# Kernel tuning notes

Measured on AMD Instinct MI355X. Metric: run time of the kernel, lower is better.

## Reference

```python
import jax, jax.numpy as jnp
import numpy as np

B, L, D, H = 8, 4096, 512, 512  # batch, seq_len, input channels, hidden_dim
EPS = 1e-5


def setup_inputs() -> dict:
    key = jax.random.key(0)
    ks = jax.random.split(key, 6)
    sD = 1.0 / np.sqrt(D)
    sH = 1.0 / np.sqrt(H)
    return {
        "x": jax.random.normal(ks[0], (B, L, D), jnp.float32),
        "ln_gamma": jnp.ones((D,), jnp.float32),
        "ln_beta": jnp.zeros((D,), jnp.float32),
        "W_B": jax.random.normal(ks[1], (D, H), jnp.float32) * sD,
        "b_B": jnp.zeros((H,), jnp.float32),
        "W_C": jax.random.normal(ks[2], (D, H), jnp.float32) * sD,
        "b_C": jnp.zeros((H,), jnp.float32),
        "W_out": jax.random.normal(ks[3], (H, H), jnp.float32) * sH,
        "b_out": jnp.zeros((H,), jnp.float32),
        # original initializes A to zeros; use decays in (0,1) for a non-trivial scan
        "A": jax.random.uniform(ks[4], (H,), jnp.float32, 0.1, 0.95),
    }


def _scan_op(e1, e2):
    # composition of affine maps h -> a*h + b (elementwise, per channel)
    a1, b1 = e1
    a2, b2 = e2
    return a1 * a2, a2 * b1 + b2


def reference(x, ln_gamma, ln_beta, W_B, b_B, W_C, b_C, W_out, b_out, A):
    # LayerNorm over channels
    mu = jnp.mean(x, axis=-1, keepdims=True)
    var = jnp.var(x, axis=-1, keepdims=True)
    xn = (x - mu) * jax.lax.rsqrt(var + EPS) * ln_gamma + ln_beta  # [B,L,D]

    Bt = jnp.einsum("bld,dh->blh", xn, W_B) + b_B  # [B,L,H]
    Ct = jnp.einsum("bld,dh->blh", xn, W_C) + b_C  # [B,L,H]

    # linear recurrence h_t = A * h_{t-1} + B_t via associative scan over L
    a_full = jnp.broadcast_to(A, Bt.shape)
    _, h = jax.lax.associative_scan(_scan_op, (a_full, Bt), axis=1)  # [B,L,H]

    y = Ct * h  # selective readout
    return jnp.einsum("blh,ho->blo", y, W_out) + b_out  # [B,L,H]
```

## Files before the change

kernel.cpp:

```cpp
#include <hip/hip_runtime.h>
#include <hip/hip_bf16.h>
#include <stdint.h>

typedef __bf16 bf16x8 __attribute__((ext_vector_type(8)));
typedef float f32x4 __attribute__((ext_vector_type(4)));

constexpr int Bn = 8, Ln = 4096, Dn = 512, Hn = 512;
constexpr int Mrows = Bn * Ln;
constexpr int CHUNK = 64, NCHUNK = Ln / CHUNK;
constexpr int LNBLK = Mrows / 4;

__global__ __launch_bounds__(256) void pre_kernel(
    const float* __restrict__ x, const float* __restrict__ gamma,
    const float* __restrict__ beta,
    const float* __restrict__ W_B, const float* __restrict__ W_C,
    const float* __restrict__ W_out, const float* __restrict__ b_B,
    const float* __restrict__ b_C,
    __hip_bfloat16* __restrict__ xn,
    __hip_bfloat16* __restrict__ WbcT, __hip_bfloat16* __restrict__ WoT,
    float* __restrict__ bbc)
{
    int t = threadIdx.x;
    if (blockIdx.x >= LNBLK) {
        int id = (blockIdx.x - LNBLK) * 256 + t;
        {
            int n = id >> 9, k = id & 511;
            float wv = (n < Hn) ? W_B[k * Hn + n] : W_C[k * Hn + (n - Hn)];
            WbcT[id] = __float2bfloat16(wv);
        }
        if (id < Hn * Hn) {
            int n = id >> 9, k = id & 511;
            WoT[id] = __float2bfloat16(W_out[k * Hn + n]);
        }
        if (id < 2 * Hn) bbc[id] = (id < Hn) ? b_B[id] : b_C[id - Hn];
        return;
    }
    int wid = t >> 6, lane = t & 63;
    int blk = blockIdx.x;
    int row = (blk & 7) * Ln + (blk >> 3) * 4 + wid;
    const float4* xr = reinterpret_cast<const float4*>(x + (size_t)row * Dn);
    float4 pa = xr[lane], pb = xr[lane + 64];
    float s  = pa.x + pa.y + pa.z + pa.w + pb.x + pb.y + pb.z + pb.w;
    float s2 = pa.x * pa.x + pa.y * pa.y + pa.z * pa.z + pa.w * pa.w
             + pb.x * pb.x + pb.y * pb.y + pb.z * pb.z + pb.w * pb.w;
    #pragma unroll
    for (int off = 1; off < 64; off <<= 1) {
        s  += __shfl_xor(s, off);
        s2 += __shfl_xor(s2, off);
    }
    float mu = s * (1.0f / Dn);
    float var = s2 * (1.0f / Dn) - mu * mu;
    float inv = rsqrtf(var + 1e-5f);
    const float4* g4 = reinterpret_cast<const float4*>(gamma);
    const float4* b4 = reinterpret_cast<const float4*>(beta);
    float4 ga = g4[lane], gb = g4[lane + 64];
    float4 ba = b4[lane], bb = b4[lane + 64];
    __hip_bfloat16 o[8];
    o[0] = __float2bfloat16((pa.x - mu) * inv * ga.x + ba.x);
    o[1] = __float2bfloat16((pa.y - mu) * inv * ga.y + ba.y);
    o[2] = __float2bfloat16((pa.z - mu) * inv * ga.z + ba.z);
    o[3] = __float2bfloat16((pa.w - mu) * inv * ga.w + ba.w);
    o[4] = __float2bfloat16((pb.x - mu) * inv * gb.x + bb.x);
    o[5] = __float2bfloat16((pb.y - mu) * inv * gb.y + bb.y);
    o[6] = __float2bfloat16((pb.z - mu) * inv * gb.z + bb.z);
    o[7] = __float2bfloat16((pb.w - mu) * inv * gb.w + bb.w);
    ushort4* xo = reinterpret_cast<ushort4*>(xn + (size_t)row * Dn);
    xo[lane]      = *reinterpret_cast<ushort4*>(&o[0]);
    xo[lane + 64] = *reinterpret_cast<ushort4*>(&o[4]);
}

template <int NT, bool OUT_BF16, bool WRITE_S>
__global__ __launch_bounds__(256, 2) void gemm4_kernel(
    const __hip_bfloat16* __restrict__ A,
    const __hip_bfloat16* __restrict__ BT,
    const float* __restrict__ bias,
    void* __restrict__ Cout,
    const float* __restrict__ Av, float* __restrict__ Sout)
{
    constexpr int K = 512, NIT = 4;
    extern __shared__ unsigned short lds[];

    int nwg = gridDim.x, bid = blockIdx.x;
    int bswz = (bid & 7) * (nwg >> 3) + (bid >> 3);
    constexpr int NBN = NT / 128;
    int bm = bswz / NBN, bnb = bswz % NBN;
    int row0 = bm * 128, col0 = bnb * 128;

    int tid = threadIdx.x;
    int w = tid >> 6, l = tid & 63;
    int rl = l & 15, qg = l >> 4;

    int scol = ((l & 7) ^ (l >> 3)) * 8;
    const __hip_bfloat16* gA = A  + (size_t)(row0 + w * 16 + (l >> 3)) * K + scol;
    const __hip_bfloat16* gB = BT + (size_t)(col0 + w * 16 + (l >> 3)) * K + scol;

#define GLDS(src, dst) __builtin_amdgcn_global_load_lds( \
        (const __attribute__((address_space(1))) void*)(const void*)(src), \
        (__attribute__((address_space(3))) void*)(void*)(dst), 16, 0, 0)
#define STA(b, kt, h, sub) GLDS(gA + (size_t)((h) * 64 + (sub) * 8) * K + (kt) * 64, \
        &lds[(b) * 16384 + (h) * 4096 + w * 1024 + (sub) * 512])
#define STB(b, kt, h, sub) GLDS(gB + (size_t)((h) * 64 + (sub) * 8) * K + (kt) * 64, \
        &lds[(b) * 16384 + 8192 + (h) * 4096 + w * 1024 + (sub) * 512])
#define STAGE_AU(b, kt, h) { STA(b, kt, h, 0); STA(b, kt, h, 1); }
#define STAGE_BU(b, kt, h) { STB(b, kt, h, 0); STB(b, kt, h, 1); }
#define BARRIER { asm volatile("" ::: "memory"); __builtin_amdgcn_s_barrier(); \
                  asm volatile("" ::: "memory"); }
#define VMCNT(n) asm volatile("s_waitcnt vmcnt(" #n ")" ::: "memory")

    int aoff = ((w >> 1) * 64 + rl) * 64;
    int boff = 8192 + ((w & 1) * 64 + rl) * 64;
    int s0k0 = (qg ^ (rl & 7)) * 8;
    int s0k1 = ((4 + qg) ^ (rl & 7)) * 8;

    f32x4 acc[4][4] = {};
    bf16x8 af[2][2], bfr[4][2];

#define RD_A(mq, b) { _Pragma("unroll") for (int i2 = 0; i2 < 2; ++i2) { \
        af[i2][0] = *(const bf16x8*)&lds[(b) * 16384 + aoff + ((mq) * 32 + i2 * 16) * 64 + s0k0]; \
        af[i2][1] = *(const bf16x8*)&lds[(b) * 16384 + aoff + ((mq) * 32 + i2 * 16) * 64 + s0k1]; } }
#define RD_B(nq, b) { _Pragma("unroll") for (int j2 = 0; j2 < 2; ++j2) { \
        bfr[(nq) * 2 + j2][0] = *(const bf16x8*)&lds[(b) * 16384 + boff + ((nq) * 32 + j2 * 16) * 64 + s0k0]; \
        bfr[(nq) * 2 + j2][1] = *(const bf16x8*)&lds[(b) * 16384 + boff + ((nq) * 32 + j2 * 16) * 64 + s0k1]; } }
#define MM2(mq) { __builtin_amdgcn_s_setprio(1); \
        _Pragma("unroll") for (int nq = 0; nq < 2; ++nq) \
        _Pragma("unroll") for (int i2 = 0; i2 < 2; ++i2) \
        _Pragma("unroll") for (int j2 = 0; j2 < 2; ++j2) \
        _Pragma("unroll") for (int kk = 0; kk < 2; ++kk) \
            acc[(mq) * 2 + i2][nq * 2 + j2] = __builtin_amdgcn_mfma_f32_16x16x32_bf16( \
                af[i2][kk], bfr[nq * 2 + j2][kk], acc[(mq) * 2 + i2][nq * 2 + j2], 0, 0, 0); \
        __builtin_amdgcn_s_setprio(0); }

    STAGE_BU(0, 0, 0); STAGE_BU(0, 0, 1); STAGE_AU(0, 0, 0); STAGE_AU(0, 0, 1);
    STAGE_BU(1, 1, 0); STAGE_BU(1, 1, 1);
    VMCNT(4);
    BARRIER;

    for (int it = 0; it < NIT; ++it) {
        int e = 2 * it;
        bool more = (it < NIT - 1);
        RD_A(0, 0); RD_B(0, 0); RD_B(1, 0);
        STAGE_AU(1, e + 1, 0); STAGE_AU(1, e + 1, 1);
        BARRIER; MM2(0); BARRIER;
        RD_A(1, 0);
        if (more) { STAGE_BU(0, e + 2, 0); STAGE_BU(0, e + 2, 1); }
        BARRIER; MM2(1);
        if (more) { VMCNT(4); } else { VMCNT(0); }
        BARRIER;
        RD_A(0, 1); RD_B(0, 1); RD_B(1, 1);
        if (more) { STAGE_AU(0, e + 2, 0); STAGE_AU(0, e + 2, 1); }
        BARRIER; MM2(0); BARRIER;
        RD_A(1, 1);
        if (more) { STAGE_BU(1, e + 3, 0); STAGE_BU(1, e + 3, 1); }
        BARRIER; MM2(1);
        if (more) { VMCNT(4); BARRIER; }
    }

    int crow0 = row0 + (w >> 1) * 64 + qg * 4;
    int ccol0 = col0 + (w & 1) * 64 + rl;
    int cg = (row0 + (w >> 1) * 64) >> 6;
    float aCol[4];
    if (WRITE_S && col0 < 512) {
        #pragma unroll
        for (int n = 0; n < 4; ++n) aCol[n] = Av[ccol0 + n * 16];
    }
    #pragma unroll
    for (int n = 0; n < 4; ++n) {
        int col = ccol0 + n * 16;
        float bv = bias[col];
        float v[4][4];
        #pragma unroll
        for (int i = 0; i < 4; ++i) {
            #pragma unroll
            for (int j = 0; j < 4; ++j) {
                v[i][j] = acc[i][n][j] + bv;
                size_t idx = (size_t)(crow0 + i * 16 + j) * NT + col;
                if (OUT_BF16)
                    ((__hip_bfloat16*)Cout)[idx] = __float2bfloat16(v[i][j]);
                else
                    ((float*)Cout)[idx] = v[i][j];
            }
        }
        if (WRITE_S && col0 < 512) {
            float a = aCol[n];
            float a2 = a * a, a4 = a2 * a2, a8 = a4 * a4, a16 = a8 * a8;
            float s = 0.f;
            #pragma unroll
            for (int i = 0; i < 4; ++i) {
                float u = ((v[i][0] * a + v[i][1]) * a + v[i][2]) * a + v[i][3];
                s = s * a16 + u;
            }
            float aq = (qg == 0) ? a8 * a4 : (qg == 1) ? a8 : (qg == 2) ? a4 : 1.0f;
            s *= aq;
            s += __shfl_xor(s, 16);
            s += __shfl_xor(s, 32);
            if (qg == 0) Sout[(size_t)cg * Hn + col] = s;
        }
    }
#undef GLDS
#undef STA
#undef STB
#undef STAGE_AU
#undef STAGE_BU
#undef BARRIER
#undef VMCNT
#undef RD_A
#undef RD_B
#undef MM2
}

__global__ __launch_bounds__(256) void scan_kernel(
    const __hip_bfloat16* __restrict__ BC, const float* __restrict__ Av,
    const float* __restrict__ S, __hip_bfloat16* __restrict__ Y)
{
    int blk = blockIdx.x;
    int b = blk & 7;
    int half = (blk >> 3) & 1;
    int c = blk >> 4;
    int hh = half * 256 + threadIdx.x;
    float a = Av[hh];
    float aG = a;
    #pragma unroll
    for (int i = 0; i < 6; ++i) aG *= aG;
    float h = 0.f;
    const float* Sp = S + (size_t)b * NCHUNK * Hn + hh;
    for (int cc = 0; cc < c; ++cc)
        h = aG * h + Sp[(size_t)cc * Hn];
    const __hip_bfloat16* p = BC + ((size_t)(b * Ln + c * CHUNK) * 1024) + hh;
    __hip_bfloat16* yp = Y + ((size_t)(b * Ln + c * CHUNK) * Hn) + hh;
    #pragma unroll 8
    for (int i = 0; i < CHUNK; ++i) {
        float bv = __bfloat162float(p[(size_t)i * 1024]);
        float cv = __bfloat162float(p[(size_t)i * 1024 + 512]);
        h = a * h + bv;
        yp[(size_t)i * Hn] = __float2bfloat16(cv * h);
    }
}

extern "C" void kernel_launch(void* const* d_in, const int* in_sizes, int n_in,
                              void* d_out, int out_size, void* d_ws, size_t ws_size,
                              hipStream_t stream)
{
    const float* x     = (const float*)d_in[0];
    const float* ln_g  = (const float*)d_in[1];
    const float* ln_b  = (const float*)d_in[2];
    const float* W_B   = (const float*)d_in[3];
    const float* b_B   = (const float*)d_in[4];
    const float* W_C   = (const float*)d_in[5];
    const float* b_C   = (const float*)d_in[6];
    const float* W_out = (const float*)d_in[7];
    const float* b_out = (const float*)d_in[8];
    const float* Avec  = (const float*)d_in[9];

    char* ws = (char*)d_ws;
    __hip_bfloat16* WbcT = (__hip_bfloat16*)(ws);
    __hip_bfloat16* WoT  = (__hip_bfloat16*)(ws + (1u << 20));
    float*          bbc  = (float*)(ws + (1u << 20) + (1u << 19));
    __hip_bfloat16* XN   = (__hip_bfloat16*)(ws + (2u << 20));
    __hip_bfloat16* BC   = (__hip_bfloat16*)(ws + (34u << 20));
    float*          Sbuf = (float*)(ws + (98u << 20));
    __hip_bfloat16* Y    = (__hip_bfloat16*)(ws + (100u << 20));

    hipFuncSetAttribute((const void*)gemm4_kernel<1024, true, true>,
                        hipFuncAttributeMaxDynamicSharedMemorySize, 65536);
    hipFuncSetAttribute((const void*)gemm4_kernel<512, false, false>,
                        hipFuncAttributeMaxDynamicSharedMemorySize, 65536);

    pre_kernel<<<LNBLK + 2048, 256, 0, stream>>>(
        x, ln_g, ln_b, W_B, W_C, W_out, b_B, b_C, XN, WbcT, WoT, bbc);
    gemm4_kernel<1024, true, true><<<(Mrows / 128) * (1024 / 128), 256, 65536, stream>>>(
        XN, WbcT, bbc, BC, Avec, Sbuf);
    scan_kernel<<<Bn * NCHUNK * 2, 256, 0, stream>>>(BC, Avec, Sbuf, Y);
    gemm4_kernel<512, false, false><<<(Mrows / 128) * (512 / 128), 256, 65536, stream>>>(
        Y, WoT, b_out, d_out, nullptr, nullptr);
}
```

Measured before the change: 121.6 us.

## Switch GEMM to K=32 double-buffered tiles with 4 waves/SIMD occupancy

Replaces the K=64 half-tile staged GEMM pipeline with a simpler loop over K=32 tiles, double-buffered in 32 KB of LDS, with one read-all/MMA-all phase per step. Halving the LDS footprint and raising launch bounds to 4 blocks per CU is meant to hide latency through occupancy rather than intra-block software pipelining. The trade-off is fewer MFMAs per barrier (16 instead of 32), more barriers overall, and possible register pressure under the tighter launch bound.

```diff
diff --git a/kernel.cpp b/kernel.cpp
--- a/kernel.cpp
+++ b/kernel.cpp
@@ -70,14 +70,14 @@
 }
 
 template <int NT, bool OUT_BF16, bool WRITE_S>
-__global__ __launch_bounds__(256, 2) void gemm4_kernel(
+__global__ __launch_bounds__(256, 4) void gemm32_kernel(
     const __hip_bfloat16* __restrict__ A,
     const __hip_bfloat16* __restrict__ BT,
     const float* __restrict__ bias,
     void* __restrict__ Cout,
     const float* __restrict__ Av, float* __restrict__ Sout)
 {
-    constexpr int K = 512, NIT = 4;
+    constexpr int K = 512, NKT = 16;
     extern __shared__ unsigned short lds[];
 
     int nwg = gridDim.x, bid = blockIdx.x;
@@ -90,69 +90,56 @@
     int w = tid >> 6, l = tid & 63;
     int rl = l & 15, qg = l >> 4;
 
-    int scol = ((l & 7) ^ (l >> 3)) * 8;
-    const __hip_bfloat16* gA = A  + (size_t)(row0 + w * 16 + (l >> 3)) * K + scol;
-    const __hip_bfloat16* gB = BT + (size_t)(col0 + w * 16 + (l >> 3)) * K + scol;
+    int srow = l >> 2, sslot = l & 3;
+    int scol = (sslot ^ (srow & 3)) * 8;
+    const __hip_bfloat16* gA = A  + (size_t)(row0 + w * 32 + srow) * K + scol;
+    const __hip_bfloat16* gB = BT + (size_t)(col0 + w * 32 + srow) * K + scol;
 
 #define GLDS(src, dst) __builtin_amdgcn_global_load_lds( \
         (const __attribute__((address_space(1))) void*)(const void*)(src), \
         (__attribute__((address_space(3))) void*)(void*)(dst), 16, 0, 0)
-#define STA(b, kt, h, sub) GLDS(gA + (size_t)((h) * 64 + (sub) * 8) * K + (kt) * 64, \
-        &lds[(b) * 16384 + (h) * 4096 + w * 1024 + (sub) * 512])
-#define STB(b, kt, h, sub) GLDS(gB + (size_t)((h) * 64 + (sub) * 8) * K + (kt) * 64, \
-        &lds[(b) * 16384 + 8192 + (h) * 4096 + w * 1024 + (sub) * 512])
-#define STAGE_AU(b, kt, h) { STA(b, kt, h, 0); STA(b, kt, h, 1); }
-#define STAGE_BU(b, kt, h) { STB(b, kt, h, 0); STB(b, kt, h, 1); }
+#define STA(b, kt, s) GLDS(gA + (size_t)(s) * 16 * K + (kt) * 32, \
+        &lds[(b) * 8192 + w * 1024 + (s) * 512])
+#define STB(b, kt, s) GLDS(gB + (size_t)(s) * 16 * K + (kt) * 32, \
+        &lds[(b) * 8192 + 4096 + w * 1024 + (s) * 512])
+#define STAGE(b, kt) { STA(b, kt, 0); STA(b, kt, 1); STB(b, kt, 0); STB(b, kt, 1); }
 #define BARRIER { asm volatile("" ::: "memory"); __builtin_amdgcn_s_barrier(); \
                   asm volatile("" ::: "memory"); }
 #define VMCNT(n) asm volatile("s_waitcnt vmcnt(" #n ")" ::: "memory")
 
-    int aoff = ((w >> 1) * 64 + rl) * 64;
-    int boff = 8192 + ((w & 1) * 64 + rl) * 64;
-    int s0k0 = (qg ^ (rl & 7)) * 8;
-    int s0k1 = ((4 + qg) ^ (rl & 7)) * 8;
+    int s0 = (qg ^ (rl & 3)) * 8;
+    int arow = (w >> 1) * 64 + rl;
+    int brow = (w & 1) * 64 + rl;
 
     f32x4 acc[4][4] = {};
-    bf16x8 af[2][2], bfr[4][2];
-
-#define RD_A(mq, b) { _Pragma("unroll") for (int i2 = 0; i2 < 2; ++i2) { \
-        af[i2][0] = *(const bf16x8*)&lds[(b) * 16384 + aoff + ((mq) * 32 + i2 * 16) * 64 + s0k0]; \
-        af[i2][1] = *(const bf16x8*)&lds[(b) * 16384 + aoff + ((mq) * 32 + i2 * 16) * 64 + s0k1]; } }
-#define RD_B(nq, b) { _Pragma("unroll") for (int j2 = 0; j2 < 2; ++j2) { \
-        bfr[(nq) * 2 + j2][0] = *(const bf16x8*)&lds[(b) * 16384 + boff + ((nq) * 32 + j2 * 16) * 64 + s0k0]; \
-        bfr[(nq) * 2 + j2][1] = *(const bf16x8*)&lds[(b) * 16384 + boff + ((nq) * 32 + j2 * 16) * 64 + s0k1]; } }
-#define MM2(mq) { __builtin_amdgcn_s_setprio(1); \
-        _Pragma("unroll") for (int nq = 0; nq < 2; ++nq) \
-        _Pragma("unroll") for (int i2 = 0; i2 < 2; ++i2) \
-        _Pragma("unroll") for (int j2 = 0; j2 < 2; ++j2) \
-        _Pragma("unroll") for (int kk = 0; kk < 2; ++kk) \
-            acc[(mq) * 2 + i2][nq * 2 + j2] = __builtin_amdgcn_mfma_f32_16x16x32_bf16( \
-                af[i2][kk], bfr[nq * 2 + j2][kk], acc[(mq) * 2 + i2][nq * 2 + j2], 0, 0, 0); \
+    bf16x8 af[4], bfr[4];
+
+#define RDALL(b) { \
+        _Pragma("unroll") for (int i2 = 0; i2 < 4; ++i2) \
+            af[i2]  = *(const bf16x8*)&lds[(b) * 8192 + (arow + i2 * 16) * 32 + s0]; \
+        _Pragma("unroll") for (int j2 = 0; j2 < 4; ++j2) \
+            bfr[j2] = *(const bf16x8*)&lds[(b) * 8192 + 4096 + (brow + j2 * 16) * 32 + s0]; }
+#define MMALL { __builtin_amdgcn_s_setprio(1); \
+        _Pragma("unroll") for (int mi = 0; mi < 4; ++mi) \
+        _Pragma("unroll") for (int ni = 0; ni < 4; ++ni) \
+            acc[mi][ni] = __builtin_amdgcn_mfma_f32_16x16x32_bf16( \
+                af[mi], bfr[ni], acc[mi][ni], 0, 0, 0); \
         __builtin_amdgcn_s_setprio(0); }
 
-    STAGE_BU(0, 0, 0); STAGE_BU(0, 0, 1); STAGE_AU(0, 0, 0); STAGE_AU(0, 0, 1);
-    STAGE_BU(1, 1, 0); STAGE_BU(1, 1, 1);
+    STAGE(0, 0); STAGE(1, 1);
     VMCNT(4);
     BARRIER;
 
-    for (int it = 0; it < NIT; ++it) {
-        int e = 2 * it;
-        bool more = (it < NIT - 1);
-        RD_A(0, 0); RD_B(0, 0); RD_B(1, 0);
-        STAGE_AU(1, e + 1, 0); STAGE_AU(1, e + 1, 1);
-        BARRIER; MM2(0); BARRIER;
-        RD_A(1, 0);
-        if (more) { STAGE_BU(0, e + 2, 0); STAGE_BU(0, e + 2, 1); }
-        BARRIER; MM2(1);
-        if (more) { VMCNT(4); } else { VMCNT(0); }
+    #pragma unroll 2
+    for (int kt = 0; kt < NKT; ++kt) {
+        int bf = kt & 1;
+        RDALL(bf);
         BARRIER;
-        RD_A(0, 1); RD_B(0, 1); RD_B(1, 1);
-        if (more) { STAGE_AU(0, e + 2, 0); STAGE_AU(0, e + 2, 1); }
-        BARRIER; MM2(0); BARRIER;
-        RD_A(1, 1);
-        if (more) { STAGE_BU(1, e + 3, 0); STAGE_BU(1, e + 3, 1); }
-        BARRIER; MM2(1);
-        if (more) { VMCNT(4); BARRIER; }
+        if (kt < NKT - 2) STAGE(bf, kt + 2);
+        MMALL;
+        if (kt < NKT - 2)      { VMCNT(4); }
+        else if (kt == NKT - 2){ VMCNT(0); }
+        BARRIER;
     }
 
     int crow0 = row0 + (w >> 1) * 64 + qg * 4;
@@ -199,13 +186,11 @@
 #undef GLDS
 #undef STA
 #undef STB
-#undef STAGE_AU
-#undef STAGE_BU
+#undef STAGE
 #undef BARRIER
 #undef VMCNT
-#undef RD_A
-#undef RD_B
-#undef MM2
+#undef RDALL
+#undef MMALL
 }
 
 __global__ __launch_bounds__(256) void scan_kernel(
@@ -260,16 +245,16 @@
     float*          Sbuf = (float*)(ws + (98u << 20));
     __hip_bfloat16* Y    = (__hip_bfloat16*)(ws + (100u << 20));
 
-    hipFuncSetAttribute((const void*)gemm4_kernel<1024, true, true>,
-                        hipFuncAttributeMaxDynamicSharedMemorySize, 65536);
-    hipFuncSetAttribute((const void*)gemm4_kernel<512, false, false>,
-                        hipFuncAttributeMaxDynamicSharedMemorySize, 65536);
+    hipFuncSetAttribute((const void*)gemm32_kernel<1024, true, true>,
+                        hipFuncAttributeMaxDynamicSharedMemorySize, 32768);
+    hipFuncSetAttribute((const void*)gemm32_kernel<512, false, false>,
+                        hipFuncAttributeMaxDynamicSharedMemorySize, 32768);
 
     pre_kernel<<<LNBLK + 2048, 256, 0, stream>>>(
         x, ln_g, ln_b, W_B, W_C, W_out, b_B, b_C, XN, WbcT, WoT, bbc);
-    gemm4_kernel<1024, true, true><<<(Mrows / 128) * (1024 / 128), 256, 65536, stream>>>(
+    gemm32_kernel<1024, true, true><<<(Mrows / 128) * (1024 / 128), 256, 32768, stream>>>(
         XN, WbcT, bbc, BC, Avec, Sbuf);
     scan_kernel<<<Bn * NCHUNK * 2, 256, 0, stream>>>(BC, Avec, Sbuf, Y);
-    gemm4_kernel<512, false, false><<<(Mrows / 128) * (512 / 128), 256, 65536, stream>>>(
+    gemm32_kernel<512, false, false><<<(Mrows / 128) * (512 / 128), 256, 32768, stream>>>(
         Y, WoT, b_out, d_out, nullptr, nullptr);
 }
```

Measured after the change: 122.7 us. No clear change (+0.9%).

## Pack BC in 4-row interleaved layout and stage fp32 output through LDS

Applied to the files above, without the earlier changes.

The first GEMM now writes its bf16 B/C output in a layout that groups 4 consecutive rows per column, so each thread stores one 8-byte ushort4 instead of four scattered 2-byte stores. The scan kernel reads that layout with vector loads, getting 4 timesteps per load. The final GEMM moves its fp32 tile through swizzled LDS in two halves so global stores become coalesced float4 rows. This is meant to reduce uncoalesced small stores and loads, at the cost of an intermediate layout the two kernels must agree on and extra barriers in the epilogue.

```diff
diff --git a/kernel.cpp b/kernel.cpp
--- a/kernel.cpp
+++ b/kernel.cpp
@@ -9,6 +9,10 @@
 constexpr int Mrows = Bn * Ln;
 constexpr int CHUNK = 64, NCHUNK = Ln / CHUNK;
 constexpr int LNBLK = Mrows / 4;
+
+static __device__ __forceinline__ unsigned short bf2u(__hip_bfloat16 x) {
+    return *reinterpret_cast<unsigned short*>(&x);
+}
 
 __global__ __launch_bounds__(256) void pre_kernel(
     const float* __restrict__ x, const float* __restrict__ gamma,
@@ -69,7 +73,7 @@
     xo[lane + 64] = *reinterpret_cast<ushort4*>(&o[4]);
 }
 
-template <int NT, bool OUT_BF16, bool WRITE_S>
+template <int NT, int OUT_MODE, bool WRITE_S>
 __global__ __launch_bounds__(256, 2) void gemm4_kernel(
     const __hip_bfloat16* __restrict__ A,
     const __hip_bfloat16* __restrict__ BT,
@@ -155,45 +159,81 @@
         if (more) { VMCNT(4); BARRIER; }
     }
 
-    int crow0 = row0 + (w >> 1) * 64 + qg * 4;
     int ccol0 = col0 + (w & 1) * 64 + rl;
     int cg = (row0 + (w >> 1) * 64) >> 6;
-    float aCol[4];
-    if (WRITE_S && col0 < 512) {
+
+    if (OUT_MODE == 0) {
+        int r4b = (row0 + (w >> 1) * 64) >> 2;
+        float aCol[4];
+        if (WRITE_S && col0 < 512) {
+            #pragma unroll
+            for (int n = 0; n < 4; ++n) aCol[n] = Av[ccol0 + n * 16];
+        }
         #pragma unroll
-        for (int n = 0; n < 4; ++n) aCol[n] = Av[ccol0 + n * 16];
-    }
-    #pragma unroll
-    for (int n = 0; n < 4; ++n) {
-        int col = ccol0 + n * 16;
-        float bv = bias[col];
-        float v[4][4];
-        #pragma unroll
-        for (int i = 0; i < 4; ++i) {
-            #pragma unroll
-            for (int j = 0; j < 4; ++j) {
-                v[i][j] = acc[i][n][j] + bv;
-                size_t idx = (size_t)(crow0 + i * 16 + j) * NT + col;
-                if (OUT_BF16)
-                    ((__hip_bfloat16*)Cout)[idx] = __float2bfloat16(v[i][j]);
-                else
-                    ((float*)Cout)[idx] = v[i][j];
-            }
-        }
-        if (WRITE_S && col0 < 512) {
-            float a = aCol[n];
-            float a2 = a * a, a4 = a2 * a2, a8 = a4 * a4, a16 = a8 * a8;
-            float s = 0.f;
+        for (int n = 0; n < 4; ++n) {
+            int col = ccol0 + n * 16;
+            float bv = bias[col];
+            float v[4][4];
             #pragma unroll
             for (int i = 0; i < 4; ++i) {
-                float u = ((v[i][0] * a + v[i][1]) * a + v[i][2]) * a + v[i][3];
-                s = s * a16 + u;
+                #pragma unroll
+                for (int j = 0; j < 4; ++j) v[i][j] = acc[i][n][j] + bv;
+                __hip_bfloat16 b0 = __float2bfloat16(v[i][0]);
+                __hip_bfloat16 b1 = __float2bfloat16(v[i][1]);
+                __hip_bfloat16 b2 = __float2bfloat16(v[i][2]);
+                __hip_bfloat16 b3 = __float2bfloat16(v[i][3]);
+                ushort4 uu;
+                uu.x = bf2u(b0); uu.y = bf2u(b1); uu.z = bf2u(b2); uu.w = bf2u(b3);
+                *reinterpret_cast<ushort4*>(
+                    (unsigned short*)Cout + ((size_t)(r4b + i * 4 + qg) * NT + col) * 4) = uu;
             }
-            float aq = (qg == 0) ? a8 * a4 : (qg == 1) ? a8 : (qg == 2) ? a4 : 1.0f;
-            s *= aq;
-            s += __shfl_xor(s, 16);
-            s += __shfl_xor(s, 32);
-            if (qg == 0) Sout[(size_t)cg * Hn + col] = s;
+            if (WRITE_S && col0 < 512) {
+                float a = aCol[n];
+                float a2 = a * a, a4 = a2 * a2, a8 = a4 * a4, a16 = a8 * a8;
+                float s = 0.f;
+                #pragma unroll
+                for (int i = 0; i < 4; ++i) {
+                    float u = ((v[i][0] * a + v[i][1]) * a + v[i][2]) * a + v[i][3];
+                    s = s * a16 + u;
+                }
+                float aq = (qg == 0) ? a8 * a4 : (qg == 1) ? a8 : (qg == 2) ? a4 : 1.0f;
+                s *= aq;
+                s += __shfl_xor(s, 16);
+                s += __shfl_xor(s, 32);
+                if (qg == 0) Sout[(size_t)cg * Hn + col] = s;
+            }
+        }
+    } else {
+        float* ldsf = (float*)lds;
+        float bv4[4];
+        #pragma unroll
+        for (int n = 0; n < 4; ++n) bv4[n] = bias[ccol0 + n * 16];
+        int halfw = (w >> 1);
+        int rl2 = tid >> 2, q = tid & 3;
+        #pragma unroll
+        for (int p = 0; p < 2; ++p) {
+            if (p) BARRIER;
+            if (halfw == p) {
+                #pragma unroll
+                for (int n = 0; n < 4; ++n)
+                    #pragma unroll
+                    for (int i = 0; i < 4; ++i)
+                        #pragma unroll
+                        for (int j = 0; j < 4; ++j) {
+                            int rloc = i * 16 + qg * 4 + j;
+                            int c = (w & 1) * 64 + n * 16 + rl;
+                            ldsf[rloc * 128 + (c ^ ((rloc & 7) << 2))] = acc[i][n][j] + bv4[n];
+                        }
+            }
+            BARRIER;
+            float* gout = (float*)Cout + (size_t)(row0 + p * 64 + rl2) * NT + col0;
+            #pragma unroll
+            for (int jj = 0; jj < 8; ++jj) {
+                int ce = q * 8 + jj;
+                float4 v4 = *reinterpret_cast<float4*>(
+                    &ldsf[rl2 * 128 + ((ce ^ (rl2 & 7)) << 2)]);
+                *reinterpret_cast<float4*>(gout + ce * 4) = v4;
+            }
         }
     }
 #undef GLDS
@@ -225,14 +265,26 @@
     const float* Sp = S + (size_t)b * NCHUNK * Hn + hh;
     for (int cc = 0; cc < c; ++cc)
         h = aG * h + Sp[(size_t)cc * Hn];
-    const __hip_bfloat16* p = BC + ((size_t)(b * Ln + c * CHUNK) * 1024) + hh;
+    const ushort4* pB = reinterpret_cast<const ushort4*>(BC)
+                        + ((size_t)((b * Ln + c * CHUNK) >> 2) * 1024 + hh);
     __hip_bfloat16* yp = Y + ((size_t)(b * Ln + c * CHUNK) * Hn) + hh;
-    #pragma unroll 8
-    for (int i = 0; i < CHUNK; ++i) {
-        float bv = __bfloat162float(p[(size_t)i * 1024]);
-        float cv = __bfloat162float(p[(size_t)i * 1024 + 512]);
-        h = a * h + bv;
-        yp[(size_t)i * Hn] = __float2bfloat16(cv * h);
+    #pragma unroll 4
+    for (int i4 = 0; i4 < 16; ++i4) {
+        ushort4 ub = pB[(size_t)i4 * 1024];
+        ushort4 uc = pB[(size_t)i4 * 1024 + 512];
+        float bv[4] = { __uint_as_float((unsigned)ub.x << 16),
+                        __uint_as_float((unsigned)ub.y << 16),
+                        __uint_as_float((unsigned)ub.z << 16),
+                        __uint_as_float((unsigned)ub.w << 16) };
+        float cv[4] = { __uint_as_float((unsigned)uc.x << 16),
+                        __uint_as_float((unsigned)uc.y << 16),
+                        __uint_as_float((unsigned)uc.z << 16),
+                        __uint_as_float((unsigned)uc.w << 16) };
+        #pragma unroll
+        for (int j = 0; j < 4; ++j) {
+            h = a * h + bv[j];
+            yp[(size_t)(i4 * 4 + j) * Hn] = __float2bfloat16(cv[j] * h);
+        }
     }
 }
 
@@ -260,16 +312,16 @@
     float*          Sbuf = (float*)(ws + (98u << 20));
     __hip_bfloat16* Y    = (__hip_bfloat16*)(ws + (100u << 20));
 
-    hipFuncSetAttribute((const void*)gemm4_kernel<1024, true, true>,
+    hipFuncSetAttribute((const void*)gemm4_kernel<1024, 0, true>,
                         hipFuncAttributeMaxDynamicSharedMemorySize, 65536);
-    hipFuncSetAttribute((const void*)gemm4_kernel<512, false, false>,
+    hipFuncSetAttribute((const void*)gemm4_kernel<512, 1, false>,
                         hipFuncAttributeMaxDynamicSharedMemorySize, 65536);
 
     pre_kernel<<<LNBLK + 2048, 256, 0, stream>>>(
         x, ln_g, ln_b, W_B, W_C, W_out, b_B, b_C, XN, WbcT, WoT, bbc);
-    gemm4_kernel<1024, true, true><<<(Mrows / 128) * (1024 / 128), 256, 65536, stream>>>(
+    gemm4_kernel<1024, 0, true><<<(Mrows / 128) * (1024 / 128), 256, 65536, stream>>>(
         XN, WbcT, bbc, BC, Avec, Sbuf);
     scan_kernel<<<Bn * NCHUNK * 2, 256, 0, stream>>>(BC, Avec, Sbuf, Y);
-    gemm4_kernel<512, false, false><<<(Mrows / 128) * (512 / 128), 256, 65536, stream>>>(
+    gemm4_kernel<512, 1, false><<<(Mrows / 128) * (512 / 128), 256, 65536, stream>>>(
         Y, WoT, b_out, d_out, nullptr, nullptr);
 }
```

Result: no change. 124.0 us (+2.0%).
